# Optimization experiments

Hardware: AMD Instinct MI355X
Metric: run time of the kernel (lower is better)

The kernel has to match this reference:

```python
import jax, jax.numpy as jnp
import numpy as np

B, N, K = 64, 128, 12
D_ATOM, D_NBR, D_NEW = 256, 320, 256
H, DK = 8, 32  # D_NEW = H * DK
LN_EPS = 1e-5
NEG_INF = -1e9


def setup_inputs() -> dict:
    key = jax.random.key(0)
    ks = jax.random.split(key, 10)
    atom_feature = jax.random.normal(ks[0], (B, N, D_ATOM), jnp.float32)
    atom_neighbor_feature = jax.random.normal(ks[1], (B, N, K, D_NBR), jnp.float32)
    # valid-neighbor masks from random neighbor counts in [1, K]
    counts = jax.random.randint(ks[2], (B, N), 1, K + 1)
    valid = (jnp.arange(K)[None, None, :] < counts[:, :, None]).astype(jnp.float32)
    atom_attend_mask = valid[..., None]                      # (B,N,K,1), 1=real neighbor
    atom_softmax_mask = (1.0 - valid[..., None]) * NEG_INF   # (B,N,K,1), additive
    # parameters
    s = 1.0 / np.sqrt(D_ATOM)
    W_atom = jax.random.uniform(ks[3], (D_ATOM, D_NEW), jnp.float32, -s, s)
    b_atom = jnp.zeros((D_NEW,), jnp.float32)
    s2 = 1.0 / np.sqrt(D_NBR)
    W_nbr = jax.random.uniform(ks[4], (D_NBR, D_NEW), jnp.float32, -s2, s2)
    b_nbr = jnp.zeros((D_NEW,), jnp.float32)
    s3 = 1.0 / np.sqrt(DK)
    w_align = jax.random.uniform(ks[5], (DK, 1), jnp.float32, -s3, s3)
    b_align = jnp.zeros((1,), jnp.float32)
    ln_gamma = jnp.ones((D_NEW,), jnp.float32)
    ln_beta = jnp.zeros((D_NEW,), jnp.float32)
    return dict(atom_feature=atom_feature, atom_neighbor_feature=atom_neighbor_feature,
                atom_softmax_mask=atom_softmax_mask, atom_attend_mask=atom_attend_mask,
                W_atom=W_atom, b_atom=b_atom, W_nbr=W_nbr, b_nbr=b_nbr,
                w_align=w_align, b_align=b_align, ln_gamma=ln_gamma, ln_beta=ln_beta)


def reference(atom_feature, atom_neighbor_feature, atom_softmax_mask, atom_attend_mask,
              W_atom, b_atom, W_nbr, b_nbr, w_align, b_align, ln_gamma, ln_beta):
    # dropout is identity at eval time
    h = atom_feature @ W_atom + b_atom                    # (B,N,D_NEW)
    e = atom_neighbor_feature @ W_nbr + b_nbr             # (B,N,K,D_NEW)
    h = h.reshape(B, N, 1, H, DK)                         # broadcast over K
    e = e.reshape(B, N, K, H, DK)
    # GATv2: act(h_i + e_j) then per-head linear score
    feat = jax.nn.leaky_relu(h + e)                       # slope 0.01 == torch default
    score = feat @ w_align + b_align                      # (B,N,K,H,1)
    score = score + atom_softmax_mask[:, :, :, None, :]   # additive -inf on pad
    attn = jax.nn.softmax(score, axis=2)                  # softmax over neighbors K
    attn = attn * atom_attend_mask[:, :, :, None, :]
    ctx = jnp.sum(attn * e, axis=2).reshape(B, N, H * DK)  # (B,N,D_NEW)
    # LayerNorm
    mu = jnp.mean(ctx, axis=-1, keepdims=True)
    xc = ctx - mu
    var = jnp.mean(xc * xc, axis=-1, keepdims=True)
    return xc * jax.lax.rsqrt(var + LN_EPS) * ln_gamma + ln_beta
```

## Files before the change

### kernel.cpp

```cpp
#include <hip/hip_runtime.h>

#define KN 12
#define DNBR 320
#define DNEW 256
#define BN_TOT 8192
#define ATB 2
#define NKS_E 10
#define NKS_H 8
#define ASTR_H 264
#define H_OFF 294912

typedef short bf8_t __attribute__((ext_vector_type(8)));
typedef float f32x4 __attribute__((ext_vector_type(4)));
typedef unsigned short us8 __attribute__((ext_vector_type(8)));
using u16 = unsigned short;
using u32 = unsigned int;

__device__ __forceinline__ u16 f2bf(float f) {
    u32 x = __float_as_uint(f);
    return (u16)((x + 0x7fffu + ((x >> 16) & 1u)) >> 16);
}

__device__ __forceinline__ us8 pack8(float4 a, float4 b) {
    us8 v;
    v[0] = f2bf(a.x); v[1] = f2bf(a.y); v[2] = f2bf(a.z); v[3] = f2bf(a.w);
    v[4] = f2bf(b.x); v[5] = f2bf(b.y); v[6] = f2bf(b.z); v[7] = f2bf(b.w);
    return v;
}

__device__ __forceinline__ bf8_t cvt8(float4 a, float4 b) {
    u32 r0, r1, r2, r3;
    asm("v_cvt_pk_bf16_f32 %0, %1, %2" : "=v"(r0) : "v"(a.x), "v"(a.y));
    asm("v_cvt_pk_bf16_f32 %0, %1, %2" : "=v"(r1) : "v"(a.z), "v"(a.w));
    asm("v_cvt_pk_bf16_f32 %0, %1, %2" : "=v"(r2) : "v"(b.x), "v"(b.y));
    asm("v_cvt_pk_bf16_f32 %0, %1, %2" : "=v"(r3) : "v"(b.z), "v"(b.w));
    union { u32 u[4]; bf8_t v; } cv;
    cv.u[0] = r0; cv.u[1] = r1; cv.u[2] = r2; cv.u[3] = r3;
    return cv.v;
}

__global__ __launch_bounds__(256) void build_b2(
    const float* __restrict__ Wn, const float* __restrict__ Wa,
    u16* __restrict__ B2)
{
    int tile = blockIdx.x * 4 + (threadIdx.x >> 6);
    int l = threadIdx.x & 63;
    int q = l >> 4, m = l & 15;
    us8 v;
    if (tile < 160) {
        int ks = tile >> 4, nt = tile & 15;
        int col = nt * 16 + m;
#pragma unroll
        for (int e = 0; e < 8; e++)
            v[e] = f2bf(Wn[(ks * 32 + q * 8 + e) * DNEW + col]);
    } else {
        int tt = tile - 160;
        int ks = tt >> 4, nt = tt & 15;
        int col = nt * 16 + m;
#pragma unroll
        for (int e = 0; e < 8; e++)
            v[e] = f2bf(Wa[(ks * 32 + q * 8 + e) * DNEW + col]);
    }
    *(us8*)&B2[(size_t)tile * 512 + l * 8] = v;
}

__global__ __launch_bounds__(256) void h_pre(
    const float* __restrict__ atomf, const u16* __restrict__ B2,
    const float* __restrict__ ba, float* __restrict__ h_g)
{
    __shared__ u16 A[32 * ASTR_H];

    const int t = threadIdx.x;
    const int l = t & 63, w = t >> 6, q = l >> 4, m = l & 15;
    const int ab = blockIdx.x * 32;

    const float* base = atomf + (size_t)ab * DNEW;
    for (int i = t; i < 1024; i += 256) {
        float4 v0 = *(const float4*)(base + i * 8);
        float4 v1 = *(const float4*)(base + i * 8 + 4);
        int a = i >> 5, c8 = i & 31;
        *(us8*)&A[a * ASTR_H + c8 * 8] = pack8(v0, v1);
    }
    __syncthreads();

    f32x4 acc[2][4];
#pragma unroll
    for (int mt = 0; mt < 2; mt++)
#pragma unroll
        for (int j = 0; j < 4; j++) acc[mt][j] = (f32x4){0.f, 0.f, 0.f, 0.f};

    for (int ks = 0; ks < NKS_H; ks++) {
        bf8_t af0 = *(bf8_t*)&A[m * ASTR_H + ks * 32 + q * 8];
        bf8_t af1 = *(bf8_t*)&A[(16 + m) * ASTR_H + ks * 32 + q * 8];
#pragma unroll
        for (int j = 0; j < 4; j++) {
            bf8_t bfj = *(const bf8_t*)&B2[((size_t)(160 + ks * 16 + w * 4 + j) * 64 + l) * 8];
            acc[0][j] = __builtin_amdgcn_mfma_f32_16x16x32_bf16(af0, bfj, acc[0][j], 0, 0, 0);
            acc[1][j] = __builtin_amdgcn_mfma_f32_16x16x32_bf16(af1, bfj, acc[1][j], 0, 0, 0);
        }
    }
#pragma unroll
    for (int mt = 0; mt < 2; mt++)
#pragma unroll
        for (int j = 0; j < 4; j++) {
            int col = w * 64 + j * 16 + m;
            float bav = ba[col];
#pragma unroll
            for (int r = 0; r < 4; r++) {
                int row = ab + mt * 16 + q * 4 + r;
                h_g[(size_t)row * DNEW + col] = acc[mt][j][r] + bav;
            }
        }
}

__global__ __launch_bounds__(256, 4) void fused_all(
    const float* __restrict__ nbrf,
    const float* __restrict__ smaskg, const float* __restrict__ amaskg,
    const u16* __restrict__ B2, const float* __restrict__ h_g,
    const float* __restrict__ bnb, const float* __restrict__ walg,
    const float* __restrict__ balg, const float* __restrict__ gam,
    const float* __restrict__ bet, float* __restrict__ out)
{
    __shared__ float red_l[ATB][8];

    const int t = threadIdx.x;
    const int l = t & 63, w = t >> 6, q = l >> 4, m = l & 15;
    const int a0 = blockIdx.x * ATB;

    const float bal = balg[0];
    float hv[ATB][4], bnbv[4], wv[4];
#pragma unroll
    for (int j = 0; j < 4; j++) {
        int col = w * 64 + j * 16 + m;
        hv[0][j] = h_g[(size_t)(a0 + 0) * DNEW + col];
        hv[1][j] = h_g[(size_t)(a0 + 1) * DNEW + col];
        bnbv[j] = bnb[col];
        wv[j] = walg[(j * 16 + m) & 31];
    }
    const bool qv = (q < 3);
    float smv[ATB][4], amv[ATB][4];
#pragma unroll
    for (int at = 0; at < ATB; at++)
#pragma unroll
        for (int r = 0; r < 4; r++) {
            int k = q * 4 + r;
            smv[at][r] = qv ? smaskg[(size_t)(a0 + at) * KN + k] + bal : 0.f;
            amv[at][r] = qv ? amaskg[(size_t)(a0 + at) * KN + k] : 0.f;
        }

    const bool mval = (m < KN);
    const float* ab0 = nbrf + ((size_t)(a0 + 0) * KN + m) * DNBR;
    const float* ab1 = nbrf + ((size_t)(a0 + 1) * KN + m) * DNBR;
    const int ko = q * 8;

    f32x4 acc_e[ATB][4];
#pragma unroll
    for (int at = 0; at < ATB; at++)
#pragma unroll
        for (int j = 0; j < 4; j++) acc_e[at][j] = (f32x4){0.f, 0.f, 0.f, 0.f};

#pragma unroll
    for (int ks = 0; ks < NKS_E; ks++) {
        bf8_t af0 = (bf8_t){0, 0, 0, 0, 0, 0, 0, 0};
        bf8_t af1 = (bf8_t){0, 0, 0, 0, 0, 0, 0, 0};
        if (mval) {
            const float* p0 = ab0 + ks * 32 + ko;
            const float* p1 = ab1 + ks * 32 + ko;
            af0 = cvt8(*(const float4*)p0, *(const float4*)(p0 + 4));
            af1 = cvt8(*(const float4*)p1, *(const float4*)(p1 + 4));
        }
#pragma unroll
        for (int j = 0; j < 4; j++) {
            bf8_t bfj = *(const bf8_t*)&B2[((size_t)(ks * 16 + w * 4 + j) * 64 + l) * 8];
            acc_e[0][j] = __builtin_amdgcn_mfma_f32_16x16x32_bf16(af0, bfj, acc_e[0][j], 0, 0, 0);
            acc_e[1][j] = __builtin_amdgcn_mfma_f32_16x16x32_bf16(af1, bfj, acc_e[1][j], 0, 0, 0);
        }
    }

#pragma unroll
    for (int j = 0; j < 4; j++) {
#pragma unroll
        for (int at = 0; at < ATB; at++)
#pragma unroll
            for (int r = 0; r < 4; r++) acc_e[at][j][r] += bnbv[j];
    }

    float ctxv[ATB][4];
#pragma unroll
    for (int at = 0; at < ATB; at++) {
        float s1 = 0.f, s2 = 0.f;
#pragma unroll
        for (int jj = 0; jj < 2; jj++) {
            float p[4];
#pragma unroll
            for (int r = 0; r < 4; r++) {
                float pp = 0.f;
#pragma unroll
                for (int jo = 0; jo < 2; jo++) {
                    int j = jj * 2 + jo;
                    float f = acc_e[at][j][r] + hv[at][j];
                    f = f > 0.f ? f : 0.01f * f;
                    pp = fmaf(f, wv[j], pp);
                }
                pp += __shfl_xor(pp, 1);
                pp += __shfl_xor(pp, 2);
                pp += __shfl_xor(pp, 4);
                pp += __shfl_xor(pp, 8);
                p[r] = qv ? pp + smv[at][r] : -1e30f;
            }
            float mx = fmaxf(fmaxf(p[0], p[1]), fmaxf(p[2], p[3]));
            mx = fmaxf(mx, __shfl_xor(mx, 16));
            mx = fmaxf(mx, __shfl_xor(mx, 32));
            float ex[4], ss = 0.f;
#pragma unroll
            for (int r = 0; r < 4; r++) {
                ex[r] = qv ? __expf(p[r] - mx) : 0.f;
                ss += ex[r];
            }
            ss += __shfl_xor(ss, 16);
            ss += __shfl_xor(ss, 32);
            float inv = 1.f / ss;
            float am[4];
#pragma unroll
            for (int r = 0; r < 4; r++)
                am[r] = qv ? ex[r] * inv * amv[at][r] : 0.f;
#pragma unroll
            for (int jo = 0; jo < 2; jo++) {
                int j = jj * 2 + jo;
                float cp = am[0] * acc_e[at][j][0] + am[1] * acc_e[at][j][1] +
                           am[2] * acc_e[at][j][2] + am[3] * acc_e[at][j][3];
                cp += __shfl_xor(cp, 16);
                cp += __shfl_xor(cp, 32);
                ctxv[at][j] = cp;
                s1 += cp;
                s2 += cp * cp;
            }
        }
#pragma unroll
        for (int off = 1; off < 16; off <<= 1) {
            s1 += __shfl_xor(s1, off);
            s2 += __shfl_xor(s2, off);
        }
        if (l == 0) { red_l[at][w] = s1; red_l[at][4 + w] = s2; }
    }
    __syncthreads();

#pragma unroll
    for (int at = 0; at < ATB; at++) {
        float ts1 = red_l[at][0] + red_l[at][1] + red_l[at][2] + red_l[at][3];
        float ts2 = red_l[at][4] + red_l[at][5] + red_l[at][6] + red_l[at][7];
        float mu = ts1 * (1.f / 256.f);
        float var = ts2 * (1.f / 256.f) - mu * mu;
        var = fmaxf(var, 0.f);
        float rs = rsqrtf(var + 1e-5f);
        if (q == 0) {
#pragma unroll
            for (int j = 0; j < 4; j++) {
                int col = w * 64 + j * 16 + m;
                out[(size_t)(a0 + at) * DNEW + col] =
                    (ctxv[at][j] - mu) * rs * gam[col] + bet[col];
            }
        }
    }
}

extern "C" void kernel_launch(void* const* d_in, const int* in_sizes, int n_in,
                              void* d_out, int out_size, void* d_ws, size_t ws_size,
                              hipStream_t stream) {
    const float* atomf = (const float*)d_in[0];
    const float* nbrf  = (const float*)d_in[1];
    const float* smask = (const float*)d_in[2];
    const float* amask = (const float*)d_in[3];
    const float* Wa    = (const float*)d_in[4];
    const float* ba    = (const float*)d_in[5];
    const float* Wn    = (const float*)d_in[6];
    const float* bnb   = (const float*)d_in[7];
    const float* wal   = (const float*)d_in[8];
    const float* bal   = (const float*)d_in[9];
    const float* gam   = (const float*)d_in[10];
    const float* bet   = (const float*)d_in[11];
    float* outp = (float*)d_out;

    u16* B2 = (u16*)d_ws;
    float* h_g = (float*)((char*)d_ws + H_OFF);

    build_b2<<<72, 256, 0, stream>>>(Wn, Wa, B2);
    h_pre<<<BN_TOT / 32, 256, 0, stream>>>(atomf, B2, ba, h_g);
    fused_all<<<BN_TOT / ATB, 256, 0, stream>>>(nbrf, smask, amask, B2, h_g,
                                                bnb, wal, bal, gam, bet, outp);
}
```

Before: 289.2 us.

## Stage neighbor features into LDS via async global_load_lds and shrink h_pre tiles

The fused kernel now copies each block's neighbor-feature rows into a 40KB shared buffer with asynchronous global-to-LDS DMA loads, issued by all four waves up front. Before this, every wave re-read the same rows from global memory inside the MFMA loop. It then reads the A fragments from LDS, converts them to bf16, and runs the MFMAs with all B fragments preloaded per k-step. Separately, h_pre processes 16 atoms per block instead of 32, doubling its grid. The large shared buffer limits blocks per CU, and the LayerNorm reduction reuses that buffer behind an extra barrier.

```diff
diff --git a/kernel.cpp b/kernel.cpp
--- a/kernel.cpp
+++ b/kernel.cpp
@@ -5,16 +5,25 @@
 #define DNEW 256
 #define BN_TOT 8192
 #define ATB 2
+#define HATB 16
 #define NKS_E 10
 #define NKS_H 8
 #define ASTR_H 264
 #define H_OFF 294912
+#define NCHUNK 40
 
 typedef short bf8_t __attribute__((ext_vector_type(8)));
 typedef float f32x4 __attribute__((ext_vector_type(4)));
 typedef unsigned short us8 __attribute__((ext_vector_type(8)));
 using u16 = unsigned short;
 using u32 = unsigned int;
+
+typedef __attribute__((address_space(3))) void lds_vp;
+typedef __attribute__((address_space(1))) const void gc_vp;
+
+__device__ __forceinline__ void dma16(const void* g, void* l) {
+    __builtin_amdgcn_global_load_lds((gc_vp*)g, (lds_vp*)l, 16, 0, 0);
+}
 
 __device__ __forceinline__ u16 f2bf(float f) {
     u32 x = __float_as_uint(f);
@@ -68,49 +77,45 @@
     const float* __restrict__ atomf, const u16* __restrict__ B2,
     const float* __restrict__ ba, float* __restrict__ h_g)
 {
-    __shared__ u16 A[32 * ASTR_H];
+    __shared__ u16 A[HATB * ASTR_H];
 
     const int t = threadIdx.x;
     const int l = t & 63, w = t >> 6, q = l >> 4, m = l & 15;
-    const int ab = blockIdx.x * 32;
+    const int ab = blockIdx.x * HATB;
 
     const float* base = atomf + (size_t)ab * DNEW;
-    for (int i = t; i < 1024; i += 256) {
-        float4 v0 = *(const float4*)(base + i * 8);
-        float4 v1 = *(const float4*)(base + i * 8 + 4);
-        int a = i >> 5, c8 = i & 31;
-        *(us8*)&A[a * ASTR_H + c8 * 8] = pack8(v0, v1);
-    }
+    float4 u0 = *(const float4*)(base + t * 8);
+    float4 u1 = *(const float4*)(base + t * 8 + 4);
+    float4 u2 = *(const float4*)(base + (t + 256) * 8);
+    float4 u3 = *(const float4*)(base + (t + 256) * 8 + 4);
+    int ai = t >> 5, c8 = t & 31;
+    *(us8*)&A[ai * ASTR_H + c8 * 8] = pack8(u0, u1);
+    *(us8*)&A[(ai + 8) * ASTR_H + c8 * 8] = pack8(u2, u3);
     __syncthreads();
 
-    f32x4 acc[2][4];
-#pragma unroll
-    for (int mt = 0; mt < 2; mt++)
-#pragma unroll
-        for (int j = 0; j < 4; j++) acc[mt][j] = (f32x4){0.f, 0.f, 0.f, 0.f};
-
+    f32x4 acc[4];
+#pragma unroll
+    for (int j = 0; j < 4; j++) acc[j] = (f32x4){0.f, 0.f, 0.f, 0.f};
+
+#pragma unroll
     for (int ks = 0; ks < NKS_H; ks++) {
-        bf8_t af0 = *(bf8_t*)&A[m * ASTR_H + ks * 32 + q * 8];
-        bf8_t af1 = *(bf8_t*)&A[(16 + m) * ASTR_H + ks * 32 + q * 8];
+        bf8_t af = *(bf8_t*)&A[m * ASTR_H + ks * 32 + q * 8];
 #pragma unroll
         for (int j = 0; j < 4; j++) {
             bf8_t bfj = *(const bf8_t*)&B2[((size_t)(160 + ks * 16 + w * 4 + j) * 64 + l) * 8];
-            acc[0][j] = __builtin_amdgcn_mfma_f32_16x16x32_bf16(af0, bfj, acc[0][j], 0, 0, 0);
-            acc[1][j] = __builtin_amdgcn_mfma_f32_16x16x32_bf16(af1, bfj, acc[1][j], 0, 0, 0);
-        }
-    }
-#pragma unroll
-    for (int mt = 0; mt < 2; mt++)
-#pragma unroll
-        for (int j = 0; j < 4; j++) {
-            int col = w * 64 + j * 16 + m;
-            float bav = ba[col];
-#pragma unroll
-            for (int r = 0; r < 4; r++) {
-                int row = ab + mt * 16 + q * 4 + r;
-                h_g[(size_t)row * DNEW + col] = acc[mt][j][r] + bav;
-            }
-        }
+            acc[j] = __builtin_amdgcn_mfma_f32_16x16x32_bf16(af, bfj, acc[j], 0, 0, 0);
+        }
+    }
+#pragma unroll
+    for (int j = 0; j < 4; j++) {
+        int col = w * 64 + j * 16 + m;
+        float bav = ba[col];
+#pragma unroll
+        for (int r = 0; r < 4; r++) {
+            int row = ab + q * 4 + r;
+            h_g[(size_t)row * DNEW + col] = acc[j][r] + bav;
+        }
+    }
 }
 
 __global__ __launch_bounds__(256, 4) void fused_all(
@@ -121,13 +126,21 @@
     const float* __restrict__ balg, const float* __restrict__ gam,
     const float* __restrict__ bet, float* __restrict__ out)
 {
-    __shared__ float red_l[ATB][8];
+    __shared__ __align__(16) float smem[NCHUNK * 256];
 
     const int t = threadIdx.x;
     const int l = t & 63, w = t >> 6, q = l >> 4, m = l & 15;
     const int a0 = blockIdx.x * ATB;
-
-    const float bal = balg[0];
+    const bool qv = (q < 3);
+
+    const int srow = (m < KN) ? m : (KN - 1);
+    for (int c = w; c < NCHUNK; c += 4) {
+        int at = c / 20, rem = c - at * 20, ksc = rem >> 1, half = rem & 1;
+        const float* src = nbrf + ((size_t)(a0 + at) * KN + srow) * DNBR
+                         + ksc * 32 + q * 8 + half * 4;
+        dma16(src, (char*)smem + (size_t)c * 1024);
+    }
+
     float hv[ATB][4], bnbv[4], wv[4];
 #pragma unroll
     for (int j = 0; j < 4; j++) {
@@ -137,7 +150,36 @@
         bnbv[j] = bnb[col];
         wv[j] = walg[(j * 16 + m) & 31];
     }
-    const bool qv = (q < 3);
+
+    __syncthreads();
+
+    const float4* A2 = (const float4*)smem;
+    f32x4 acc_e[ATB][4];
+#pragma unroll
+    for (int at = 0; at < ATB; at++)
+#pragma unroll
+        for (int j = 0; j < 4; j++) acc_e[at][j] = (f32x4){0.f, 0.f, 0.f, 0.f};
+
+#pragma unroll
+    for (int ks = 0; ks < NKS_E; ks++) {
+        bf8_t bfj[4];
+#pragma unroll
+        for (int j = 0; j < 4; j++)
+            bfj[j] = *(const bf8_t*)&B2[((size_t)(ks * 16 + w * 4 + j) * 64 + l) * 8];
+        float4 lo0 = A2[(size_t)((0 * NKS_E + ks) * 2 + 0) * 64 + l];
+        float4 hi0 = A2[(size_t)((0 * NKS_E + ks) * 2 + 1) * 64 + l];
+        float4 lo1 = A2[(size_t)((1 * NKS_E + ks) * 2 + 0) * 64 + l];
+        float4 hi1 = A2[(size_t)((1 * NKS_E + ks) * 2 + 1) * 64 + l];
+        bf8_t af0 = cvt8(lo0, hi0);
+        bf8_t af1 = cvt8(lo1, hi1);
+#pragma unroll
+        for (int j = 0; j < 4; j++) {
+            acc_e[0][j] = __builtin_amdgcn_mfma_f32_16x16x32_bf16(af0, bfj[j], acc_e[0][j], 0, 0, 0);
+            acc_e[1][j] = __builtin_amdgcn_mfma_f32_16x16x32_bf16(af1, bfj[j], acc_e[1][j], 0, 0, 0);
+        }
+    }
+
+    const float bal = balg[0];
     float smv[ATB][4], amv[ATB][4];
 #pragma unroll
     for (int at = 0; at < ATB; at++)
@@ -148,35 +190,6 @@
             amv[at][r] = qv ? amaskg[(size_t)(a0 + at) * KN + k] : 0.f;
         }
 
-    const bool mval = (m < KN);
-    const float* ab0 = nbrf + ((size_t)(a0 + 0) * KN + m) * DNBR;
-    const float* ab1 = nbrf + ((size_t)(a0 + 1) * KN + m) * DNBR;
-    const int ko = q * 8;
-
-    f32x4 acc_e[ATB][4];
-#pragma unroll
-    for (int at = 0; at < ATB; at++)
-#pragma unroll
-        for (int j = 0; j < 4; j++) acc_e[at][j] = (f32x4){0.f, 0.f, 0.f, 0.f};
-
-#pragma unroll
-    for (int ks = 0; ks < NKS_E; ks++) {
-        bf8_t af0 = (bf8_t){0, 0, 0, 0, 0, 0, 0, 0};
-        bf8_t af1 = (bf8_t){0, 0, 0, 0, 0, 0, 0, 0};
-        if (mval) {
-            const float* p0 = ab0 + ks * 32 + ko;
-            const float* p1 = ab1 + ks * 32 + ko;
-            af0 = cvt8(*(const float4*)p0, *(const float4*)(p0 + 4));
-            af1 = cvt8(*(const float4*)p1, *(const float4*)(p1 + 4));
-        }
-#pragma unroll
-        for (int j = 0; j < 4; j++) {
-            bf8_t bfj = *(const bf8_t*)&B2[((size_t)(ks * 16 + w * 4 + j) * 64 + l) * 8];
-            acc_e[0][j] = __builtin_amdgcn_mfma_f32_16x16x32_bf16(af0, bfj, acc_e[0][j], 0, 0, 0);
-            acc_e[1][j] = __builtin_amdgcn_mfma_f32_16x16x32_bf16(af1, bfj, acc_e[1][j], 0, 0, 0);
-        }
-    }
-
 #pragma unroll
     for (int j = 0; j < 4; j++) {
 #pragma unroll
@@ -185,7 +198,7 @@
             for (int r = 0; r < 4; r++) acc_e[at][j][r] += bnbv[j];
     }
 
-    float ctxv[ATB][4];
+    float ctxv[ATB][4], s1s[ATB], s2s[ATB];
 #pragma unroll
     for (int at = 0; at < ATB; at++) {
         float s1 = 0.f, s2 = 0.f;
@@ -241,14 +254,24 @@
             s1 += __shfl_xor(s1, off);
             s2 += __shfl_xor(s2, off);
         }
-        if (l == 0) { red_l[at][w] = s1; red_l[at][4 + w] = s2; }
-    }
+        s1s[at] = s1; s2s[at] = s2;
+    }
+
+    float* red_l = smem;
     __syncthreads();
+    if (l == 0) {
+#pragma unroll
+        for (int at = 0; at < ATB; at++) {
+            red_l[at * 8 + w] = s1s[at];
+            red_l[at * 8 + 4 + w] = s2s[at];
+        }
+    }
+    __syncthreads();
 
 #pragma unroll
     for (int at = 0; at < ATB; at++) {
-        float ts1 = red_l[at][0] + red_l[at][1] + red_l[at][2] + red_l[at][3];
-        float ts2 = red_l[at][4] + red_l[at][5] + red_l[at][6] + red_l[at][7];
+        float ts1 = red_l[at * 8 + 0] + red_l[at * 8 + 1] + red_l[at * 8 + 2] + red_l[at * 8 + 3];
+        float ts2 = red_l[at * 8 + 4] + red_l[at * 8 + 5] + red_l[at * 8 + 6] + red_l[at * 8 + 7];
         float mu = ts1 * (1.f / 256.f);
         float var = ts2 * (1.f / 256.f) - mu * mu;
         var = fmaxf(var, 0.f);
@@ -285,7 +308,7 @@
     float* h_g = (float*)((char*)d_ws + H_OFF);
 
     build_b2<<<72, 256, 0, stream>>>(Wn, Wa, B2);
-    h_pre<<<BN_TOT / 32, 256, 0, stream>>>(atomf, B2, ba, h_g);
+    h_pre<<<BN_TOT / HATB, 256, 0, stream>>>(atomf, B2, ba, h_g);
     fused_all<<<BN_TOT / ATB, 256, 0, stream>>>(nbrf, smask, amask, B2, h_g,
                                                 bnb, wal, bal, gam, bet, outp);
 }
```

Result: faster. 251.1 us (-13.2%).
